# Kernel optimization log

Measured on AMD Instinct MI355X. Metric: run time of the kernel, lower is better.

The kernel has to match this reference:

```python
import jax, jax.numpy as jnp
import numpy as np

B = 2 ** 21          # batch of independent 3-qubit state vectors
NQ = 3               # qubits, state dim = 2**NQ = 8
INV_SQRT2 = np.float32(1.0 / np.sqrt(2.0))


def setup_inputs() -> dict:
    key = jax.random.key(0)
    k1, k2, k3, k4 = jax.random.split(key, 4)
    x_real = jax.random.normal(k1, (B, 8), jnp.float32)
    x_imag = jax.random.normal(k2, (B, 8), jnp.float32)
    theta = jax.random.normal(k3, (2,), jnp.float32)   # learned RX angles for qubits 0,1
    angle = jax.random.normal(k4, (1,), jnp.float32)   # dead arg (R built but never applied)
    return {"x_real": x_real, "x_imag": x_imag, "theta": theta, "angle": angle}


def _apply_1q(x, U, qubit):
    # x: (B,2,2,2) complex state, U: (2,2) gate, qubit in {0,1,2} -> axis qubit+1
    x = jnp.moveaxis(x, qubit + 1, -1)
    x = jnp.einsum('...j,ij->...i', x, U)
    return jnp.moveaxis(x, -1, qubit + 1)


def _circuit(x_real, x_imag, theta):
    x = (x_real + 1j * x_imag).astype(jnp.complex64).reshape(-1, 2, 2, 2)
    # Hadamard on qubits 0 and 1
    H = jnp.array([[1.0, 1.0], [1.0, -1.0]], jnp.complex64) * INV_SQRT2
    x = _apply_1q(x, H, 0)
    x = _apply_1q(x, H, 1)
    # RX(theta_q) = exp(-i theta sigma_x / 2) on qubits 0 and 1
    for q in (0, 1):
        c = jnp.cos(theta[q] * 0.5).astype(jnp.complex64)
        s = jnp.sin(theta[q] * 0.5).astype(jnp.complex64)
        RX = jnp.stack([jnp.stack([c, -1j * s]), jnp.stack([-1j * s, c])])
        x = _apply_1q(x, RX, q)
    # CNOT: control=qubit 0, target=qubit 2 (flip target axis when control=1)
    x = jnp.stack([x[:, 0], x[:, 1, :, ::-1]], axis=1)
    x = x.reshape(-1, 8)
    return jnp.stack([jnp.real(x), jnp.imag(x)], axis=-1)  # (B, 8, 2) float32


def reference(x_real, x_imag, theta, angle):
    # `angle` is dead code in the original forward (R created, never applied)
    return _circuit(x_real, x_imag, theta)
```

## Files before the change

kernel.cpp:

```cpp
#include <hip/hip_runtime.h>

__global__ __launch_bounds__(256) void circuit_kernel(
    const float4* __restrict__ xr4,
    const float4* __restrict__ xi4,
    const float* __restrict__ theta,
    float4* __restrict__ o4,
    int N)
{
    int u = blockIdx.x * blockDim.x + threadIdx.x;
    if (u >= N) return;
    const int h = u & 1;
    const float k = 0.70710678118654752440f;

    float c0, s0, c1, s1;
    __sincosf(theta[0] * 0.5f, &s0, &c0);
    __sincosf(theta[1] * 0.5f, &s1, &c1);

    const float mr = k * c0;
    const float mi = h ? (k * s0) : (-k * s0);

    float4 fr = xr4[u];
    float4 fi = xi4[u];
    float ar[4] = {fr.x, fr.y, fr.z, fr.w};
    float ai[4] = {fi.x, fi.y, fi.z, fi.w};

    float lr[4], li[4], pr[4], pi[4];
#pragma unroll
    for (int j = 0; j < 4; ++j) {
        lr[j] = mr * ar[j] - mi * ai[j];
        li[j] = mr * ai[j] + mi * ar[j];
    }
#pragma unroll
    for (int j = 0; j < 4; ++j) {
        pr[j] = __shfl_xor(lr[j], 1, 64);
        pi[j] = __shfl_xor(li[j], 1, 64);
    }
#pragma unroll
    for (int j = 0; j < 4; ++j) {
        ar[j] = h ? (pr[j] - lr[j]) : (lr[j] + pr[j]);
        ai[j] = h ? (pi[j] - li[j]) : (li[j] + pi[j]);
    }

    const float p1r = k * c1, p1i = -k * s1;
    const float q1r = k * c1, q1i = k * s1;
#pragma unroll
    for (int j = 0; j < 2; ++j) {
        float xr_ = p1r * ar[j]     - p1i * ai[j];
        float xi_ = p1r * ai[j]     + p1i * ar[j];
        float yr_ = q1r * ar[j + 2] - q1i * ai[j + 2];
        float yi_ = q1r * ai[j + 2] + q1i * ar[j + 2];
        ar[j]     = xr_ + yr_;  ai[j]     = xi_ + yi_;
        ar[j + 2] = xr_ - yr_;  ai[j + 2] = xi_ - yi_;
    }

    int a = h ? 1 : 0, b = h ? 0 : 1, c = h ? 3 : 2, d = h ? 2 : 3;
    o4[2 * u]     = make_float4(ar[a], ai[a], ar[b], ai[b]);
    o4[2 * u + 1] = make_float4(ar[c], ai[c], ar[d], ai[d]);
}

extern "C" void kernel_launch(void* const* d_in, const int* in_sizes, int n_in,
                              void* d_out, int out_size, void* d_ws, size_t ws_size,
                              hipStream_t stream) {
    const float4* xr4  = (const float4*)d_in[0];
    const float4* xi4  = (const float4*)d_in[1];
    const float* theta = (const float*)d_in[2];
    float4* o4 = (float4*)d_out;

    int N = in_sizes[0] / 4;
    int block = 256;
    int grid = (N + block - 1) / block;
    circuit_kernel<<<grid, block, 0, stream>>>(xr4, xi4, theta, o4, N);
}
```

Measured before the change: 239.0 us.

## Process whole states per thread with batched loads, drop cross-lane shuffles

Each thread now handles one full 8-amplitude state instead of half a state, so the qubit-0 gate no longer needs wavefront shuffles. Each thread batches four states, issuing all loads before compute to raise memory-level parallelism. The grid shrinks by a factor of K. The trade-off is strided 32-byte per-thread accesses in place of contiguous 16-byte ones, plus higher register use from holding four states at once.

```diff
diff --git a/kernel.cpp b/kernel.cpp
--- a/kernel.cpp
+++ b/kernel.cpp
@@ -1,61 +1,83 @@
 #include <hip/hip_runtime.h>
+
+
+__device__ __forceinline__ void state_compute_store(
+    float4 fr0, float4 fr1, float4 fi0, float4 fi1,
+    float kc0, float ks0, float kc1, float ks1,
+    float4* __restrict__ o4, int s)
+{
+    float r[8]  = {fr0.x, fr0.y, fr0.z, fr0.w, fr1.x, fr1.y, fr1.z, fr1.w};
+    float im[8] = {fi0.x, fi0.y, fi0.z, fi0.w, fi1.x, fi1.y, fi1.z, fi1.w};
+
+#pragma unroll
+    for (int j = 0; j < 4; ++j) {
+        float ar = r[j], ai = im[j], br = r[j + 4], bi = im[j + 4];
+        float par = kc0 * ar + ks0 * ai;
+        float pai = kc0 * ai - ks0 * ar;
+        float qbr = kc0 * br - ks0 * bi;
+        float qbi = kc0 * bi + ks0 * br;
+        r[j]      = par + qbr;  im[j]     = pai + qbi;
+        r[j + 4]  = par - qbr;  im[j + 4] = pai - qbi;
+    }
+
+#pragma unroll
+    for (int t = 0; t < 4; ++t) {
+        int j = (t & 1) + ((t & 2) << 1);
+        float ar = r[j], ai = im[j], br = r[j + 2], bi = im[j + 2];
+        float par = kc1 * ar + ks1 * ai;
+        float pai = kc1 * ai - ks1 * ar;
+        float qbr = kc1 * br - ks1 * bi;
+        float qbi = kc1 * bi + ks1 * br;
+        r[j]      = par + qbr;  im[j]     = pai + qbi;
+        r[j + 2]  = par - qbr;  im[j + 2] = pai - qbi;
+    }
+
+    o4[4 * s + 0] = make_float4(r[0], im[0], r[1], im[1]);
+    o4[4 * s + 1] = make_float4(r[2], im[2], r[3], im[3]);
+    o4[4 * s + 2] = make_float4(r[5], im[5], r[4], im[4]);
+    o4[4 * s + 3] = make_float4(r[7], im[7], r[6], im[6]);
+}
 
 __global__ __launch_bounds__(256) void circuit_kernel(
     const float4* __restrict__ xr4,
     const float4* __restrict__ xi4,
     const float* __restrict__ theta,
     float4* __restrict__ o4,
-    int N)
+    int S)
 {
-    int u = blockIdx.x * blockDim.x + threadIdx.x;
-    if (u >= N) return;
-    const int h = u & 1;
+    constexpr int K = 4;
     const float k = 0.70710678118654752440f;
 
-    float c0, s0, c1, s1;
-    __sincosf(theta[0] * 0.5f, &s0, &c0);
-    __sincosf(theta[1] * 0.5f, &s1, &c1);
+    float c0, s0v, c1, s1v;
+    __sincosf(theta[0] * 0.5f, &s0v, &c0);
+    __sincosf(theta[1] * 0.5f, &s1v, &c1);
+    const float kc0 = k * c0, ks0 = k * s0v;
+    const float kc1 = k * c1, ks1 = k * s1v;
 
-    const float mr = k * c0;
-    const float mi = h ? (k * s0) : (-k * s0);
+    const int tid = blockIdx.x * blockDim.x + threadIdx.x;
+    const int T   = gridDim.x * blockDim.x;
 
-    float4 fr = xr4[u];
-    float4 fi = xi4[u];
-    float ar[4] = {fr.x, fr.y, fr.z, fr.w};
-    float ai[4] = {fi.x, fi.y, fi.z, fi.w};
-
-    float lr[4], li[4], pr[4], pi[4];
+    if (tid + (K - 1) * T < S) {
+        float4 R0[K], R1[K], I0[K], I1[K];
 #pragma unroll
-    for (int j = 0; j < 4; ++j) {
-        lr[j] = mr * ar[j] - mi * ai[j];
-        li[j] = mr * ai[j] + mi * ar[j];
+        for (int m = 0; m < K; ++m) {
+            int s = tid + m * T;
+            R0[m] = xr4[2 * s];  R1[m] = xr4[2 * s + 1];
+            I0[m] = xi4[2 * s];  I1[m] = xi4[2 * s + 1];
+        }
+#pragma unroll
+        for (int m = 0; m < K; ++m) {
+            state_compute_store(R0[m], R1[m], I0[m], I1[m],
+                                kc0, ks0, kc1, ks1, o4, tid + m * T);
+        }
+    } else {
+        for (int s = tid; s < S; s += T) {
+            float4 r0 = xr4[2 * s], r1 = xr4[2 * s + 1];
+            float4 i0 = xi4[2 * s], i1 = xi4[2 * s + 1];
+            state_compute_store(r0, r1, i0, i1,
+                                kc0, ks0, kc1, ks1, o4, s);
+        }
     }
-#pragma unroll
-    for (int j = 0; j < 4; ++j) {
-        pr[j] = __shfl_xor(lr[j], 1, 64);
-        pi[j] = __shfl_xor(li[j], 1, 64);
-    }
-#pragma unroll
-    for (int j = 0; j < 4; ++j) {
-        ar[j] = h ? (pr[j] - lr[j]) : (lr[j] + pr[j]);
-        ai[j] = h ? (pi[j] - li[j]) : (li[j] + pi[j]);
-    }
-
-    const float p1r = k * c1, p1i = -k * s1;
-    const float q1r = k * c1, q1i = k * s1;
-#pragma unroll
-    for (int j = 0; j < 2; ++j) {
-        float xr_ = p1r * ar[j]     - p1i * ai[j];
-        float xi_ = p1r * ai[j]     + p1i * ar[j];
-        float yr_ = q1r * ar[j + 2] - q1i * ai[j + 2];
-        float yi_ = q1r * ai[j + 2] + q1i * ar[j + 2];
-        ar[j]     = xr_ + yr_;  ai[j]     = xi_ + yi_;
-        ar[j + 2] = xr_ - yr_;  ai[j + 2] = xi_ - yi_;
-    }
-
-    int a = h ? 1 : 0, b = h ? 0 : 1, c = h ? 3 : 2, d = h ? 2 : 3;
-    o4[2 * u]     = make_float4(ar[a], ai[a], ar[b], ai[b]);
-    o4[2 * u + 1] = make_float4(ar[c], ai[c], ar[d], ai[d]);
 }
 
 extern "C" void kernel_launch(void* const* d_in, const int* in_sizes, int n_in,
@@ -66,8 +88,9 @@
     const float* theta = (const float*)d_in[2];
     float4* o4 = (float4*)d_out;
 
-    int N = in_sizes[0] / 4;
+    int S = in_sizes[0] / 8;
+    const int K = 4;
     int block = 256;
-    int grid = (N + block - 1) / block;
-    circuit_kernel<<<grid, block, 0, stream>>>(xr4, xi4, theta, o4, N);
+    int grid = (S + K * block - 1) / (K * block);
+    circuit_kernel<<<grid, block, 0, stream>>>(xr4, xi4, theta, o4, S);
 }
```

Result: slower. 251.3 us (+5.1%).

## Use persistent grid-stride loop with prefetch, LDS-staged coalesced nontemporal stores

Applied to the files above, without the earlier changes.

Launches a fixed grid of 2048 blocks that loops over the batch, prefetching the next iteration's inputs while computing the current one. Results are staged in a double-buffered shared-memory tile and written back with contiguous nontemporal stores. This aims to improve store coalescing, avoid cache pollution from the write-only output, and hide load latency. It adds a block barrier per iteration and shared-memory traffic.

```diff
diff --git a/kernel.cpp b/kernel.cpp
--- a/kernel.cpp
+++ b/kernel.cpp
@@ -1,61 +1,88 @@
 #include <hip/hip_runtime.h>
+
+
+typedef float float4_n __attribute__((ext_vector_type(4)));
 
 __global__ __launch_bounds__(256) void circuit_kernel(
     const float4* __restrict__ xr4,
     const float4* __restrict__ xi4,
     const float* __restrict__ theta,
     float4* __restrict__ o4,
-    int N)
+    int N,
+    int niters)
 {
-    int u = blockIdx.x * blockDim.x + threadIdx.x;
-    if (u >= N) return;
-    const int h = u & 1;
+    __shared__ float4 buf[2][512];
+    const int tid = threadIdx.x;
+    const int stride = gridDim.x * blockDim.x;
+    const int h = tid & 1;
     const float k = 0.70710678118654752440f;
 
     float c0, s0, c1, s1;
     __sincosf(theta[0] * 0.5f, &s0, &c0);
     __sincosf(theta[1] * 0.5f, &s1, &c1);
-
-    const float mr = k * c0;
-    const float mi = h ? (k * s0) : (-k * s0);
-
-    float4 fr = xr4[u];
-    float4 fi = xi4[u];
-    float ar[4] = {fr.x, fr.y, fr.z, fr.w};
-    float ai[4] = {fi.x, fi.y, fi.z, fi.w};
-
-    float lr[4], li[4], pr[4], pi[4];
-#pragma unroll
-    for (int j = 0; j < 4; ++j) {
-        lr[j] = mr * ar[j] - mi * ai[j];
-        li[j] = mr * ai[j] + mi * ar[j];
-    }
-#pragma unroll
-    for (int j = 0; j < 4; ++j) {
-        pr[j] = __shfl_xor(lr[j], 1, 64);
-        pi[j] = __shfl_xor(li[j], 1, 64);
-    }
-#pragma unroll
-    for (int j = 0; j < 4; ++j) {
-        ar[j] = h ? (pr[j] - lr[j]) : (lr[j] + pr[j]);
-        ai[j] = h ? (pi[j] - li[j]) : (li[j] + pi[j]);
-    }
-
+    const float mr  = k * c0;
+    const float mi  = h ? (k * s0) : (-k * s0);
     const float p1r = k * c1, p1i = -k * s1;
     const float q1r = k * c1, q1i = k * s1;
+
+    int u = blockIdx.x * blockDim.x + tid;
+    float4 fr = make_float4(0.f, 0.f, 0.f, 0.f), fi = fr;
+    if (u < N) { fr = xr4[u]; fi = xi4[u]; }
+    int par = 0;
+
+    for (int it = 0; it < niters; ++it) {
+        const int un = u + stride;
+        float4 frn = make_float4(0.f, 0.f, 0.f, 0.f), fin = frn;
+        if (it + 1 < niters && un < N) { frn = xr4[un]; fin = xi4[un]; }
+
+        float ar[4] = {fr.x, fr.y, fr.z, fr.w};
+        float ai[4] = {fi.x, fi.y, fi.z, fi.w};
+        float lr[4], li[4], pr[4], pi[4];
 #pragma unroll
-    for (int j = 0; j < 2; ++j) {
-        float xr_ = p1r * ar[j]     - p1i * ai[j];
-        float xi_ = p1r * ai[j]     + p1i * ar[j];
-        float yr_ = q1r * ar[j + 2] - q1i * ai[j + 2];
-        float yi_ = q1r * ai[j + 2] + q1i * ar[j + 2];
-        ar[j]     = xr_ + yr_;  ai[j]     = xi_ + yi_;
-        ar[j + 2] = xr_ - yr_;  ai[j + 2] = xi_ - yi_;
+        for (int j = 0; j < 4; ++j) {
+            lr[j] = mr * ar[j] - mi * ai[j];
+            li[j] = mr * ai[j] + mi * ar[j];
+        }
+#pragma unroll
+        for (int j = 0; j < 4; ++j) {
+            pr[j] = __shfl_xor(lr[j], 1, 64);
+            pi[j] = __shfl_xor(li[j], 1, 64);
+        }
+#pragma unroll
+        for (int j = 0; j < 4; ++j) {
+            ar[j] = h ? (pr[j] - lr[j]) : (lr[j] + pr[j]);
+            ai[j] = h ? (pi[j] - li[j]) : (li[j] + pi[j]);
+        }
+
+#pragma unroll
+        for (int j = 0; j < 2; ++j) {
+            float xr_ = p1r * ar[j]     - p1i * ai[j];
+            float xi_ = p1r * ai[j]     + p1i * ar[j];
+            float yr_ = q1r * ar[j + 2] - q1i * ai[j + 2];
+            float yi_ = q1r * ai[j + 2] + q1i * ar[j + 2];
+            ar[j]     = xr_ + yr_;  ai[j]     = xi_ + yi_;
+            ar[j + 2] = xr_ - yr_;  ai[j + 2] = xi_ - yi_;
+        }
+
+        const int a = h ? 1 : 0, b = h ? 0 : 1, c = h ? 3 : 2, d = h ? 2 : 3;
+        buf[par][2 * tid]     = make_float4(ar[a], ai[a], ar[b], ai[b]);
+        buf[par][2 * tid + 1] = make_float4(ar[c], ai[c], ar[d], ai[d]);
+        __syncthreads();
+
+        const long gbase = 2L * (long)(u - tid);
+        float4_n* __restrict__ dst = (float4_n*)(o4 + gbase);
+        const float4_n* __restrict__ src = (const float4_n*)buf[par];
+        const long lim = 2L * (long)N;
+        if (gbase + tid < lim)
+            __builtin_nontemporal_store(src[tid], &dst[tid]);
+        if (gbase + tid + 256 < lim)
+            __builtin_nontemporal_store(src[tid + 256], &dst[tid + 256]);
+
+        par ^= 1;
+        u = un;
+        fr = frn;
+        fi = fin;
     }
-
-    int a = h ? 1 : 0, b = h ? 0 : 1, c = h ? 3 : 2, d = h ? 2 : 3;
-    o4[2 * u]     = make_float4(ar[a], ai[a], ar[b], ai[b]);
-    o4[2 * u + 1] = make_float4(ar[c], ai[c], ar[d], ai[d]);
 }
 
 extern "C" void kernel_launch(void* const* d_in, const int* in_sizes, int n_in,
@@ -68,6 +95,8 @@
 
     int N = in_sizes[0] / 4;
     int block = 256;
-    int grid = (N + block - 1) / block;
-    circuit_kernel<<<grid, block, 0, stream>>>(xr4, xi4, theta, o4, N);
+    int grid  = 2048;
+    int stride = grid * block;
+    int niters = (N + stride - 1) / stride;
+    circuit_kernel<<<grid, block, 0, stream>>>(xr4, xi4, theta, o4, N, niters);
 }
```

Result: no change. 239.2 us (+0.1%).
